# Kernel optimization log

Measured on AMD Instinct MI355X. Metric: run time of the kernel, lower is better.

The kernel has to match this reference:

```python
import jax, jax.numpy as jnp
import numpy as np

NUM_HEADS = 8
BLOCK = 8      # block_size
HALO = 2       # kernel_size (halo width)


def _rel_to_abs(rel):
    # halo-style relative->absolute conversion
    # rel: [B, G, qh, qw, 2*p-1] -> [B, G, qh, qw, p]
    B, G, qh, qw, dim = rel.shape
    p = (dim + 1) // 2
    gap = p - qw
    flat = rel.reshape(B, G, qh, qw * dim)[:, :, :, qw - 1:-1]
    return flat.reshape(B, G, qh, qw, 2 * (p - 1))[:, :, :, :, gap:p + gap]


def _relative_logits(pos_q, pos_emb_h, pos_emb_w):
    # pos_q: [B, G, qb, qb, kd]; pos_emb_*: [kd, 2*p-1]
    rel_w = _rel_to_abs(jnp.einsum('bghwd,dr->bghwr', pos_q, pos_emb_w))  # [B,G,qb,qb,p] key-width
    q_t = pos_q.transpose(0, 1, 3, 2, 4)
    rel_h = _rel_to_abs(jnp.einsum('bgwhd,dr->bgwhr', q_t, pos_emb_h))
    rel_h = rel_h.transpose(0, 1, 3, 2, 4)  # [B,G,qb,qb,p] key-height
    return rel_h[..., :, None] + rel_w[..., None, :]  # [B,G,qb,qb,p,p]


def reference(x, w_q, w_kv, w_out, pos_emb_h, pos_emb_w):
    B, H, W, C = x.shape
    kd = C // NUM_HEADS                # per-head key dim
    kvk = BLOCK + 2 * HALO             # halo window size
    out_ch = w_out.shape[1]
    v_dim = out_ch // NUM_HEADS
    kv_per_head = (C + out_ch) // NUM_HEADS
    hh, ww = H // BLOCK, W // BLOCK
    scale = float(1.0 / np.sqrt(kd))

    # ---- query (1x1 conv == matmul), blockify ----
    q = (x @ w_q).reshape(B, hh, BLOCK, ww, BLOCK, NUM_HEADS, kd)
    q = q.transpose(0, 5, 1, 3, 2, 4, 6)  # [B,nh,hh,ww,qb,qb,kd]
    attn_q = q.reshape(B, NUM_HEADS, hh, ww, BLOCK * BLOCK, kd) * scale
    pos_q = q.reshape(B, NUM_HEADS * hh * ww, BLOCK, BLOCK, kd)

    # ---- key/value: 1x1 conv, halo pad, unfold into overlapping windows ----
    kv = jnp.pad(x @ w_kv, ((0, 0), (HALO, HALO), (HALO, HALO), (0, 0)))
    idx = np.arange(hh)[:, None] * BLOCK + np.arange(kvk)[None, :]  # [hh,kvk]
    idy = np.arange(ww)[:, None] * BLOCK + np.arange(kvk)[None, :]  # [ww,kvk]
    patches = kv[:, idx][:, :, :, idy]           # [B,hh,kvk,ww,kvk,kv_dim]
    patches = patches.transpose(0, 1, 3, 2, 4, 5)  # [B,hh,ww,kvk,kvk,kv_dim]
    kvh = patches.reshape(B, hh, ww, kvk, kvk, NUM_HEADS, kv_per_head)
    kvh = kvh.transpose(0, 5, 1, 2, 3, 4, 6).reshape(B, NUM_HEADS, hh, ww, kvk * kvk, kv_per_head)
    key, value = kvh[..., :kd], kvh[..., kd:]

    # ---- attention with relative position bias ----
    scores = jnp.einsum('bnhwqd,bnhwkd->bnhwqk', attn_q, key)
    pos = _relative_logits(pos_q, pos_emb_h, pos_emb_w)
    pos = pos.reshape(B, NUM_HEADS, hh, ww, BLOCK * BLOCK, kvk * kvk)
    attn = jax.nn.softmax(scores + pos, axis=-1)
    out = jnp.einsum('bnhwqk,bnhwkv->bnhwqv', attn, value)  # [B,nh,hh,ww,qb*qb,v_dim]

    # ---- de-blockify, output projection ----
    out = out.reshape(B, NUM_HEADS, hh, ww, BLOCK, BLOCK, v_dim)
    out = out.transpose(0, 2, 4, 3, 5, 1, 6).reshape(B, H, W, NUM_HEADS * v_dim)
    return out @ w_out


def setup_inputs() -> dict:
    key = jax.random.key(0)
    ks = jax.random.split(key, 6)
    B, H, W, C = 4, 128, 128, 256
    out_ch = 256
    kd = C // NUM_HEADS
    kvk = BLOCK + 2 * HALO
    std = kd ** -0.5
    return {
        'x': jax.random.normal(ks[0], (B, H, W, C), jnp.float32),
        'w_q': jax.random.normal(ks[1], (C, C), jnp.float32) * 0.02,
        'w_kv': jax.random.normal(ks[2], (C, C + out_ch), jnp.float32) * 0.02,
        'w_out': jax.random.normal(ks[3], (C, out_ch), jnp.float32) * 0.02,
        'pos_emb_h': jax.random.normal(ks[4], (kd, 2 * kvk - 1), jnp.float32) * std,
        'pos_emb_w': jax.random.normal(ks[5], (kd, 2 * kvk - 1), jnp.float32) * std,
    }
```

## Files before the change

kernel.cpp:

```cpp
#include <hip/hip_runtime.h>
#include <hip/hip_bf16.h>
#include <cstdint>


#define KVK 12
#define NKEYS 144
#define VT_S 160
#define PT_S 168
#define LOG2E 1.4426950408889634f

typedef unsigned int u32;
typedef unsigned long long u64;
typedef unsigned short u16;
typedef __attribute__((ext_vector_type(8))) __bf16 bf16x8;
typedef __attribute__((ext_vector_type(4))) float f32x4;

__device__ __forceinline__ u16 f2bf(float f) {
    u32 x = __float_as_uint(f);
    return (u16)((x + 0x7fffu + ((x >> 16) & 1u)) >> 16);
}
__device__ __forceinline__ u32 cvtpk(float lo, float hi) {
    u32 d;
    asm("v_cvt_pk_bf16_f32 %0, %1, %2" : "=v"(d) : "v"(lo), "v"(hi));
    return d;
}
__device__ __forceinline__ float max3f(float a, float b, float c) {
    float d;
    asm("v_max3_f32 %0, %1, %2, %3" : "=v"(d) : "v"(a), "v"(b), "v"(c));
    return d;
}
__device__ __forceinline__ float exp2a(float x) {
    float d;
    asm("v_exp_f32 %0, %1" : "=v"(d) : "v"(x));
    return d;
}
__device__ __forceinline__ void gload16(const void* g, void* l) {
    __builtin_amdgcn_global_load_lds(
        (const __attribute__((address_space(1))) void*)g,
        (__attribute__((address_space(3))) void*)l, 16, 0, 0);
}
__device__ __forceinline__ u32 pack2(float lo, float hi) {
    return (u32)f2bf(lo) | ((u32)f2bf(hi) << 16);
}

__global__ __launch_bounds__(256) void conv_prep(const float* __restrict__ x,
                                                 u16* __restrict__ xb,
                                                 const float* __restrict__ wq,
                                                 const float* __restrict__ wkv,
                                                 const float* __restrict__ wout,
                                                 u16* __restrict__ wT,
                                                 u16* __restrict__ woutT,
                                                 const float* __restrict__ emb_h,
                                                 const float* __restrict__ emb_w,
                                                 u16* __restrict__ embT) {
    int blk = blockIdx.x, t = threadIdx.x;
    if (blk < 8192) {
        int i = blk * 256 + t;
        const float4* p = reinterpret_cast<const float4*>(x) + (long)i * 2;
        float4 a = p[0], b = p[1];
        uint4 o;
        o.x = pack2(a.x, a.y); o.y = pack2(a.z, a.w);
        o.z = pack2(b.x, b.y); o.w = pack2(b.z, b.w);
        reinterpret_cast<uint4*>(xb)[i] = o;
        return;
    }
    blk -= 8192;
    if (blk < 256) {
        int idx = blk * 256 + t; int nn = idx >> 8, k = idx & 255;
        wT[idx] = f2bf(wq[(long)k * 256 + nn]);
    } else if (blk < 768) {
        int idx = (blk - 256) * 256 + t; int nn = idx >> 8, k = idx & 255;
        float v = wkv[(long)k * 512 + nn];
        if ((nn & 32) == 0) v *= 0.2550348642f;
        wT[65536 + idx] = f2bf(v);
    } else if (blk < 1024) {
        int idx = (blk - 768) * 256 + t; int nn = idx >> 8, k = idx & 255;
        woutT[idx] = f2bf(wout[(long)k * 256 + nn]);
    } else if (blk == 1024) {
        for (int i = t; i < 1024; i += 256) {
            int p = i >> 5, d = i & 31;
            embT[i] = (p < 23) ? f2bf(emb_h[d * 23 + p]) : 0;
        }
    } else {
        for (int i = t; i < 1024; i += 256) {
            int p = i >> 5, d = i & 31;
            embT[1024 + i] = (p < 23) ? f2bf(emb_w[d * 23 + p]) : 0;
        }
    }
}

__global__ __launch_bounds__(256) void gemm_qkv6(const u16* __restrict__ A,
                                                 const u16* __restrict__ WT,
                                                 u16* __restrict__ Qb,
                                                 u16* __restrict__ KVb) {
    __shared__ u16 As[8192];
    __shared__ u16 Bs[8192];
    const int t = threadIdx.x;
    const int bid = blockIdx.x;
    const int mIdx = (bid / 48) * 8 + (bid & 7);
    const int nt = (bid >> 3) % 6;
    const int w = t >> 6, lane = t & 63;
    const long m0 = (long)mIdx * 128;
    const long n0 = (long)nt * 128;
    const int wr = w >> 1, wc = w & 1;
    const int r = lane & 15, g = lane >> 4;

    f32x4 acc[4][4];
    #pragma unroll
    for (int i = 0; i < 4; ++i)
        #pragma unroll
        for (int j = 0; j < 4; ++j) acc[i][j] = (f32x4){0.f, 0.f, 0.f, 0.f};

    const u16* Ags[4];
    const u16* Bgs[4];
    #pragma unroll
    for (int cq = 0; cq < 4; ++cq) {
        int u = cq * 256 + w * 64 + lane;
        int panel = u >> 9, row = (u >> 2) & 127, col8 = (u & 3) * 8;
        Ags[cq] = A + (m0 + row) * 256 + panel * 32 + col8;
        Bgs[cq] = WT + (n0 + row) * 256 + panel * 32 + col8;
    }

    for (int k0 = 0; k0 < 256; k0 += 64) {
        #pragma unroll
        for (int cq = 0; cq < 4; ++cq) {
            gload16(Ags[cq] + k0, &As[cq * 2048 + w * 512]);
            gload16(Bgs[cq] + k0, &Bs[cq * 2048 + w * 512]);
        }
        __syncthreads();
        #pragma unroll
        for (int kk = 0; kk < 2; ++kk) {
            bf16x8 a[4], b[4];
            #pragma unroll
            for (int i = 0; i < 4; ++i)
                a[i] = *reinterpret_cast<const bf16x8*>(
                    &As[kk * 4096 + (wr * 64 + i * 16 + r) * 32 + g * 8]);
            #pragma unroll
            for (int j = 0; j < 4; ++j)
                b[j] = *reinterpret_cast<const bf16x8*>(
                    &Bs[kk * 4096 + (wc * 64 + j * 16 + r) * 32 + g * 8]);
            #pragma unroll
            for (int i = 0; i < 4; ++i)
                #pragma unroll
                for (int j = 0; j < 4; ++j)
                    acc[i][j] = __builtin_amdgcn_mfma_f32_16x16x32_bf16(b[j], a[i], acc[i][j], 0, 0, 0);
        }
        __syncthreads();
    }

    const bool isQ = (nt < 2);
    #pragma unroll
    for (int i = 0; i < 4; ++i) {
        long row = m0 + wr * 64 + i * 16 + r;
        #pragma unroll
        for (int j = 0; j < 4; ++j) {
            long colb = n0 + wc * 64 + j * 16 + g * 4;
            uint2 st;
            st.x = cvtpk(acc[i][j][0], acc[i][j][1]);
            st.y = cvtpk(acc[i][j][2], acc[i][j][3]);
            if (isQ) *reinterpret_cast<uint2*>(Qb + row * 256 + colb) = st;
            else     *reinterpret_cast<uint2*>(KVb + row * 512 + colb - 256) = st;
        }
    }
}

__global__ __launch_bounds__(256) void mfma_gemm(const u16* __restrict__ A,
                                                 const u16* __restrict__ BT,
                                                 float* __restrict__ C, int N) {
    __shared__ u16 As[8192];
    __shared__ u16 Bs[8192];
    const int t = threadIdx.x;
    const int bid = blockIdx.x;
    const int mIdx = (bid / 16) * 8 + (bid & 7);
    const int nt = (bid >> 3) & 1;
    const int w = t >> 6, lane = t & 63;
    const long m0 = (long)mIdx * 128;
    const long n0 = (long)nt * 128;
    const int wr = w >> 1, wc = w & 1;
    const int r = lane & 15, g = lane >> 4;

    f32x4 acc[4][4];
    #pragma unroll
    for (int i = 0; i < 4; ++i)
        #pragma unroll
        for (int j = 0; j < 4; ++j) acc[i][j] = (f32x4){0.f, 0.f, 0.f, 0.f};

    const u16* Ags[4];
    const u16* Bgs[4];
    #pragma unroll
    for (int cq = 0; cq < 4; ++cq) {
        int u = cq * 256 + w * 64 + lane;
        int panel = u >> 9, row = (u >> 2) & 127, col8 = (u & 3) * 8;
        Ags[cq] = A + (m0 + row) * 256 + panel * 32 + col8;
        Bgs[cq] = BT + (n0 + row) * 256 + panel * 32 + col8;
    }

    for (int k0 = 0; k0 < 256; k0 += 64) {
        #pragma unroll
        for (int cq = 0; cq < 4; ++cq) {
            gload16(Ags[cq] + k0, &As[cq * 2048 + w * 512]);
            gload16(Bgs[cq] + k0, &Bs[cq * 2048 + w * 512]);
        }
        __syncthreads();
        #pragma unroll
        for (int kk = 0; kk < 2; ++kk) {
            bf16x8 a[4], b[4];
            #pragma unroll
            for (int i = 0; i < 4; ++i)
                a[i] = *reinterpret_cast<const bf16x8*>(
                    &As[kk * 4096 + (wr * 64 + i * 16 + r) * 32 + g * 8]);
            #pragma unroll
            for (int j = 0; j < 4; ++j)
                b[j] = *reinterpret_cast<const bf16x8*>(
                    &Bs[kk * 4096 + (wc * 64 + j * 16 + r) * 32 + g * 8]);
            #pragma unroll
            for (int i = 0; i < 4; ++i)
                #pragma unroll
                for (int j = 0; j < 4; ++j)
                    acc[i][j] = __builtin_amdgcn_mfma_f32_16x16x32_bf16(b[j], a[i], acc[i][j], 0, 0, 0);
        }
        __syncthreads();
    }

    #pragma unroll
    for (int i = 0; i < 4; ++i) {
        long row = m0 + wr * 64 + i * 16 + r;
        #pragma unroll
        for (int j = 0; j < 4; ++j) {
            long colb = n0 + wc * 64 + j * 16 + g * 4;
            float4 st = make_float4(acc[i][j][0], acc[i][j][1], acc[i][j][2], acc[i][j][3]);
            *reinterpret_cast<float4*>(C + row * N + colb) = st;
        }
    }
}

__global__ __launch_bounds__(256, 5) void attn_mfma(const u16* __restrict__ Qb,
                                                    const u16* __restrict__ KVb,
                                                    const u16* __restrict__ embT,
                                                    u16* __restrict__ Ob) {
    __shared__ __align__(16) char blob[22528];
    u16* Ks  = (u16*)blob;
    u16* Qe  = (u16*)(blob + 18432);
    u16* PT  = (u16*)blob;
    __shared__ u16 Vt[32 * VT_S];

    const int gblk = blockIdx.x;
    const int n = gblk & 7;
    const int bx = (gblk >> 3) & 15;
    const int by = (gblk >> 7) & 15;
    const int b = gblk >> 11;
    const int t = threadIdx.x;
    const int w = t >> 6, lane = t & 63;
    const int g = lane >> 4, r = lane & 15;

    const int q = w * 16 + r;
    const int qi = q >> 3, qj = q & 7;
    const long qrow = ((long)b * 128 + by * 8 + qi) * 128 + bx * 8 + qj;

    bf16x8 qa1 = *reinterpret_cast<const bf16x8*>(Qb + qrow * 256 + n * 32 + g * 8);

    for (int u = t; u < NKEYS * 8; u += 256) {
        int kk = u >> 3, part = u & 7;
        int ky = kk / KVK, kx = kk - ky * KVK;
        int gy = by * 8 + ky - 2, gx = bx * 8 + kx - 2;
        uint4 val = make_uint4(0u, 0u, 0u, 0u);
        if ((unsigned)gy < 128u && (unsigned)gx < 128u) {
            long row = ((long)b * 128 + gy) * 128 + gx;
            val = *reinterpret_cast<const uint4*>(KVb + row * 512 + n * 64 + part * 8);
        }
        if (part < 4) {
            int col = (part * 8) ^ ((kk & 7) << 3);
            *reinterpret_cast<uint4*>(&Ks[kk * 64 + col]) = val;
        } else {
            int d0 = (part - 4) * 8;
            u16 tmp[8];
            *reinterpret_cast<uint4*>(tmp) = val;
            #pragma unroll
            for (int i = 0; i < 8; ++i) {
                int d = d0 + i;
                Vt[d * VT_S + (kk ^ (((d >> 3) & 3) << 3))] = tmp[i];
            }
        }
    }
    for (int u = t; u < 576; u += 256) {
        int kk = u >> 2, uu = u & 3;
        int ky = (kk * 171) >> 11;
        int kx = kk - 12 * ky;
        int hy = ky - 8 * uu;
        int hx = 12 + kx - 8 * uu;
        u64 lo = 0, hi = 0;
        if ((unsigned)hy < 4u) lo |= 0x3F80ULL << (hy * 16);
        else if ((unsigned)hy < 8u) hi |= 0x3F80ULL << ((hy - 4) * 16);
        if ((unsigned)hx < 4u) lo |= 0x3F80ULL << (hx * 16);
        else if ((unsigned)hx < 8u) hi |= 0x3F80ULL << ((hx - 4) * 16);
        int col = (32 + uu * 8) ^ ((kk & 7) << 3);
        u64* dst = reinterpret_cast<u64*>(&Ks[kk * 64 + col]);
        dst[0] = lo;
        dst[1] = hi;
    }
    if (t < 64) *reinterpret_cast<uint4*>(&Qe[t * 32 + 24]) = make_uint4(0u, 0u, 0u, 0u);
    if (t >= 224) {
        int d = t - 224;
        int sw = ((d >> 3) & 3) << 3;
        *reinterpret_cast<uint4*>(&Vt[d * VT_S + (144 ^ sw)]) = make_uint4(0u, 0u, 0u, 0u);
        *reinterpret_cast<uint4*>(&Vt[d * VT_S + (152 ^ sw)]) = make_uint4(0u, 0u, 0u, 0u);
    }

    {
        bf16x8 ah0 = *reinterpret_cast<const bf16x8*>(embT + r * 32 + g * 8);
        bf16x8 ah1 = *reinterpret_cast<const bf16x8*>(embT + (16 + r) * 32 + g * 8);
        bf16x8 aw0 = *reinterpret_cast<const bf16x8*>(embT + 1024 + r * 32 + g * 8);
        bf16x8 aw1 = *reinterpret_cast<const bf16x8*>(embT + 1024 + (16 + r) * 32 + g * 8);
        f32x4 z = (f32x4){0.f, 0.f, 0.f, 0.f};
        f32x4 rh0 = __builtin_amdgcn_mfma_f32_16x16x32_bf16(ah0, qa1, z, 0, 0, 0);
        f32x4 rh1 = __builtin_amdgcn_mfma_f32_16x16x32_bf16(ah1, qa1, z, 0, 0, 0);
        f32x4 rw0 = __builtin_amdgcn_mfma_f32_16x16x32_bf16(aw0, qa1, z, 0, 0, 0);
        f32x4 rw1 = __builtin_amdgcn_mfma_f32_16x16x32_bf16(aw1, qa1, z, 0, 0, 0);
        #pragma unroll
        for (int ti = 0; ti < 2; ++ti) {
            #pragma unroll
            for (int e = 0; e < 4; ++e) {
                int p = ti * 16 + g * 4 + e;
                float vh = (ti ? rh1[e] : rh0[e]) * LOG2E;
                float vw = (ti ? rw1[e] : rw0[e]) * LOG2E;
                int kyd = p + qi - 11;
                int kxd = p + qj - 11;
                if ((unsigned)kyd < 12u) Qe[q * 32 + kyd] = f2bf(vh);
                if ((unsigned)kxd < 12u) Qe[q * 32 + 12 + kxd] = f2bf(vw);
            }
        }
    }
    __syncthreads();

    bf16x8 qa2 = *reinterpret_cast<const bf16x8*>(&Qe[q * 32 + g * 8]);
    f32x4 acc[9];
    #pragma unroll
    for (int j = 0; j < 9; ++j) {
        int krow = j * 16 + r;
        int sw = (r & 7) << 3;
        bf16x8 kb0 = *reinterpret_cast<const bf16x8*>(&Ks[krow * 64 + ((g * 8) ^ sw)]);
        bf16x8 kb1 = *reinterpret_cast<const bf16x8*>(&Ks[krow * 64 + ((32 + g * 8) ^ sw)]);
        f32x4 z = (f32x4){0.f, 0.f, 0.f, 0.f};
        acc[j] = __builtin_amdgcn_mfma_f32_16x16x32_bf16(kb1, qa2,
                 __builtin_amdgcn_mfma_f32_16x16x32_bf16(kb0, qa1, z, 0, 0, 0), 0, 0, 0);
    }

    float mx = max3f(acc[0][0], acc[0][1], acc[0][2]);
    mx = fmaxf(mx, acc[0][3]);
    #pragma unroll
    for (int j = 1; j < 9; ++j)
        mx = max3f(mx, max3f(acc[j][0], acc[j][1], acc[j][2]), acc[j][3]);
    mx = fmaxf(mx, __shfl_xor(mx, 16));
    mx = fmaxf(mx, __shfl_xor(mx, 32));
    float s0 = 0.f, s1 = 0.f, s2 = 0.f, s3 = 0.f;
    u32 pkA[9], pkB[9];
    #pragma unroll
    for (int j = 0; j < 9; ++j) {
        float e0 = exp2a(acc[j][0] - mx);
        float e1 = exp2a(acc[j][1] - mx);
        float e2 = exp2a(acc[j][2] - mx);
        float e3 = exp2a(acc[j][3] - mx);
        s0 += e0; s1 += e1; s2 += e2; s3 += e3;
        pkA[j] = cvtpk(e0, e1);
        pkB[j] = cvtpk(e2, e3);
    }
    float sum = (s0 + s1) + (s2 + s3);
    sum += __shfl_xor(sum, 16);
    sum += __shfl_xor(sum, 32);
    const float inv = __builtin_amdgcn_rcpf(sum);

    __syncthreads();

    {
        const int ptb = q * PT_S;
        #pragma unroll
        for (int j = 0; j < 9; ++j) {
            *reinterpret_cast<u32*>(&PT[ptb + 16 * j + 4 * g]) = pkA[j];
            *reinterpret_cast<u32*>(&PT[ptb + 16 * j + 4 * g + 2]) = pkB[j];
        }
    }
    if (t < 64) {
        *reinterpret_cast<uint4*>(&PT[t * PT_S + 144]) = make_uint4(0u, 0u, 0u, 0u);
        *reinterpret_cast<uint4*>(&PT[t * PT_S + 152]) = make_uint4(0u, 0u, 0u, 0u);
    }
    __syncthreads();

    const int sw0 = (r >> 3) << 3;
    const int sw1 = (2 + (r >> 3)) << 3;
    f32x4 o0 = (f32x4){0.f, 0.f, 0.f, 0.f};
    f32x4 o1 = (f32x4){0.f, 0.f, 0.f, 0.f};
    #pragma unroll
    for (int kk = 0; kk < 5; ++kk) {
        bf16x8 pb = *reinterpret_cast<const bf16x8*>(&PT[q * PT_S + kk * 32 + g * 8]);
        bf16x8 va0 = *reinterpret_cast<const bf16x8*>(&Vt[r * VT_S + ((kk * 32 + g * 8) ^ sw0)]);
        bf16x8 va1 = *reinterpret_cast<const bf16x8*>(&Vt[(16 + r) * VT_S + ((kk * 32 + g * 8) ^ sw1)]);
        o0 = __builtin_amdgcn_mfma_f32_16x16x32_bf16(va0, pb, o0, 0, 0, 0);
        o1 = __builtin_amdgcn_mfma_f32_16x16x32_bf16(va1, pb, o1, 0, 0, 0);
    }
    {
        uint2 st0, st1;
        st0.x = cvtpk(o0[0] * inv, o0[1] * inv);
        st0.y = cvtpk(o0[2] * inv, o0[3] * inv);
        st1.x = cvtpk(o1[0] * inv, o1[1] * inv);
        st1.y = cvtpk(o1[2] * inv, o1[3] * inv);
        *reinterpret_cast<uint2*>(Ob + qrow * 256 + n * 32 + g * 4) = st0;
        *reinterpret_cast<uint2*>(Ob + qrow * 256 + n * 32 + 16 + g * 4) = st1;
    }
}

extern "C" void kernel_launch(void* const* d_in, const int* in_sizes, int n_in,
                              void* d_out, int out_size, void* d_ws, size_t ws_size,
                              hipStream_t stream) {
    const float* x     = (const float*)d_in[0];
    const float* w_q   = (const float*)d_in[1];
    const float* w_kv  = (const float*)d_in[2];
    const float* w_out = (const float*)d_in[3];
    const float* emb_h = (const float*)d_in[4];
    const float* emb_w = (const float*)d_in[5];

    u16* xb = (u16*)d_out;
    u16* Qb = (u16*)((char*)d_out + (size_t)33554432);
    char* ws = (char*)d_ws;
    u16* KVb   = (u16*)(ws);
    u16* Ob    = (u16*)(ws + (size_t)67108864);
    u16* wT    = (u16*)(ws + (size_t)100663296);
    u16* woutT = (u16*)(ws + (size_t)100663296 + 393216);
    u16* embT  = (u16*)(ws + (size_t)100663296 + 524288);

    dim3 blk(256);
    conv_prep<<<dim3(9218), blk, 0, stream>>>(x, xb, w_q, w_kv, w_out, wT, woutT,
                                              emb_h, emb_w, embT);
    gemm_qkv6<<<dim3(3072), blk, 0, stream>>>(xb, wT, Qb, KVb);
    attn_mfma<<<dim3(8192), blk, 0, stream>>>(Qb, KVb, embT, Ob);
    mfma_gemm<<<dim3(1024), blk, 0, stream>>>(Ob, woutT, (float*)d_out, 256);
}
```

Measured before the change: 146.5 us.

## Issue all KV gathers up front and defer V scatter behind positional MFMAs

The KV window load is restructured so each thread issues all its global loads (key and value halves together) up front into registers, stores K immediately, and defers the V transpose-scatter until after the relative-position MFMA work. The embedding loads are hoisted to the kernel start. s_setprio brackets are added around the MFMA sections so waves doing matrix math get scheduling priority. The goal is to hide global-load latency behind independent compute; the cost is more live registers under a launch bound of 5 blocks per SM.

```diff
diff --git a/kernel.cpp b/kernel.cpp
--- a/kernel.cpp
+++ b/kernel.cpp
@@ -234,6 +234,25 @@
     }
 }
 
+#define UNITLOAD(U, VK, VV, KD, VB) {                                          \
+    int kk_ = (U) >> 2, p_ = (U) & 3;                                          \
+    int ky_ = (kk_ * 171) >> 11, kx_ = kk_ - 12 * ky_;                         \
+    int gy_ = by * 8 + ky_ - 2, gx_ = bx * 8 + kx_ - 2;                        \
+    if (((unsigned)gy_ < 128u) && ((unsigned)gx_ < 128u)) {                    \
+        const u16* bp_ = KVb + (((long)b * 128 + gy_) * 128 + gx_) * 512 + n * 64 + p_ * 8; \
+        VK = *reinterpret_cast<const uint4*>(bp_);                             \
+        VV = *reinterpret_cast<const uint4*>(bp_ + 32);                        \
+    }                                                                          \
+    KD = kk_ * 64 + ((p_ * 8) ^ ((kk_ & 7) << 3));                             \
+    VB = (p_ * 8) * VT_S + (kk_ ^ (p_ << 3));                                  \
+}
+#define VSCAT(VV, VB) {                                                        \
+    u16 tmp_[8];                                                               \
+    *reinterpret_cast<uint4*>(tmp_) = VV;                                      \
+    _Pragma("unroll")                                                          \
+    for (int i_ = 0; i_ < 8; ++i_) Vt[(VB) + i_ * VT_S] = tmp_[i_];            \
+}
+
 __global__ __launch_bounds__(256, 5) void attn_mfma(const u16* __restrict__ Qb,
                                                     const u16* __restrict__ KVb,
                                                     const u16* __restrict__ embT,
@@ -258,30 +277,22 @@
     const long qrow = ((long)b * 128 + by * 8 + qi) * 128 + bx * 8 + qj;
 
     bf16x8 qa1 = *reinterpret_cast<const bf16x8*>(Qb + qrow * 256 + n * 32 + g * 8);
-
-    for (int u = t; u < NKEYS * 8; u += 256) {
-        int kk = u >> 3, part = u & 7;
-        int ky = kk / KVK, kx = kk - ky * KVK;
-        int gy = by * 8 + ky - 2, gx = bx * 8 + kx - 2;
-        uint4 val = make_uint4(0u, 0u, 0u, 0u);
-        if ((unsigned)gy < 128u && (unsigned)gx < 128u) {
-            long row = ((long)b * 128 + gy) * 128 + gx;
-            val = *reinterpret_cast<const uint4*>(KVb + row * 512 + n * 64 + part * 8);
-        }
-        if (part < 4) {
-            int col = (part * 8) ^ ((kk & 7) << 3);
-            *reinterpret_cast<uint4*>(&Ks[kk * 64 + col]) = val;
-        } else {
-            int d0 = (part - 4) * 8;
-            u16 tmp[8];
-            *reinterpret_cast<uint4*>(tmp) = val;
-            #pragma unroll
-            for (int i = 0; i < 8; ++i) {
-                int d = d0 + i;
-                Vt[d * VT_S + (kk ^ (((d >> 3) & 3) << 3))] = tmp[i];
-            }
-        }
-    }
+    bf16x8 ah0 = *reinterpret_cast<const bf16x8*>(embT + r * 32 + g * 8);
+    bf16x8 ah1 = *reinterpret_cast<const bf16x8*>(embT + (16 + r) * 32 + g * 8);
+    bf16x8 aw0 = *reinterpret_cast<const bf16x8*>(embT + 1024 + r * 32 + g * 8);
+    bf16x8 aw1 = *reinterpret_cast<const bf16x8*>(embT + 1024 + (16 + r) * 32 + g * 8);
+
+    uint4 z4 = make_uint4(0u, 0u, 0u, 0u);
+    uint4 vK0 = z4, vV0 = z4, vK1 = z4, vV1 = z4, vK2 = z4, vV2 = z4;
+    int kd0 = 0, vb0 = 0, kd1 = 0, vb1 = 0, kd2 = 0, vb2 = 0;
+    UNITLOAD(t, vK0, vV0, kd0, vb0);
+    UNITLOAD(t + 256, vK1, vV1, kd1, vb1);
+    if (t < 64) UNITLOAD(t + 512, vK2, vV2, kd2, vb2);
+
+    *reinterpret_cast<uint4*>(&Ks[kd0]) = vK0;
+    *reinterpret_cast<uint4*>(&Ks[kd1]) = vK1;
+    if (t < 64) *reinterpret_cast<uint4*>(&Ks[kd2]) = vK2;
+
     for (int u = t; u < 576; u += 256) {
         int kk = u >> 2, uu = u & 3;
         int ky = (kk * 171) >> 11;
@@ -298,24 +309,22 @@
         dst[0] = lo;
         dst[1] = hi;
     }
-    if (t < 64) *reinterpret_cast<uint4*>(&Qe[t * 32 + 24]) = make_uint4(0u, 0u, 0u, 0u);
+    if (t < 64) *reinterpret_cast<uint4*>(&Qe[t * 32 + 24]) = z4;
     if (t >= 224) {
         int d = t - 224;
         int sw = ((d >> 3) & 3) << 3;
-        *reinterpret_cast<uint4*>(&Vt[d * VT_S + (144 ^ sw)]) = make_uint4(0u, 0u, 0u, 0u);
-        *reinterpret_cast<uint4*>(&Vt[d * VT_S + (152 ^ sw)]) = make_uint4(0u, 0u, 0u, 0u);
+        *reinterpret_cast<uint4*>(&Vt[d * VT_S + (144 ^ sw)]) = z4;
+        *reinterpret_cast<uint4*>(&Vt[d * VT_S + (152 ^ sw)]) = z4;
     }
 
     {
-        bf16x8 ah0 = *reinterpret_cast<const bf16x8*>(embT + r * 32 + g * 8);
-        bf16x8 ah1 = *reinterpret_cast<const bf16x8*>(embT + (16 + r) * 32 + g * 8);
-        bf16x8 aw0 = *reinterpret_cast<const bf16x8*>(embT + 1024 + r * 32 + g * 8);
-        bf16x8 aw1 = *reinterpret_cast<const bf16x8*>(embT + 1024 + (16 + r) * 32 + g * 8);
         f32x4 z = (f32x4){0.f, 0.f, 0.f, 0.f};
+        __builtin_amdgcn_s_setprio(1);
         f32x4 rh0 = __builtin_amdgcn_mfma_f32_16x16x32_bf16(ah0, qa1, z, 0, 0, 0);
         f32x4 rh1 = __builtin_amdgcn_mfma_f32_16x16x32_bf16(ah1, qa1, z, 0, 0, 0);
         f32x4 rw0 = __builtin_amdgcn_mfma_f32_16x16x32_bf16(aw0, qa1, z, 0, 0, 0);
         f32x4 rw1 = __builtin_amdgcn_mfma_f32_16x16x32_bf16(aw1, qa1, z, 0, 0, 0);
+        __builtin_amdgcn_s_setprio(0);
         #pragma unroll
         for (int ti = 0; ti < 2; ++ti) {
             #pragma unroll
@@ -330,10 +339,16 @@
             }
         }
     }
+
+    VSCAT(vV0, vb0);
+    VSCAT(vV1, vb1);
+    if (t < 64) VSCAT(vV2, vb2);
+
     __syncthreads();
 
     bf16x8 qa2 = *reinterpret_cast<const bf16x8*>(&Qe[q * 32 + g * 8]);
     f32x4 acc[9];
+    __builtin_amdgcn_s_setprio(1);
     #pragma unroll
     for (int j = 0; j < 9; ++j) {
         int krow = j * 16 + r;
@@ -344,6 +359,7 @@
         acc[j] = __builtin_amdgcn_mfma_f32_16x16x32_bf16(kb1, qa2,
                  __builtin_amdgcn_mfma_f32_16x16x32_bf16(kb0, qa1, z, 0, 0, 0), 0, 0, 0);
     }
+    __builtin_amdgcn_s_setprio(0);
 
     float mx = max3f(acc[0][0], acc[0][1], acc[0][2]);
     mx = fmaxf(mx, acc[0][3]);
@@ -389,6 +405,7 @@
     const int sw1 = (2 + (r >> 3)) << 3;
     f32x4 o0 = (f32x4){0.f, 0.f, 0.f, 0.f};
     f32x4 o1 = (f32x4){0.f, 0.f, 0.f, 0.f};
+    __builtin_amdgcn_s_setprio(1);
     #pragma unroll
     for (int kk = 0; kk < 5; ++kk) {
         bf16x8 pb = *reinterpret_cast<const bf16x8*>(&PT[q * PT_S + kk * 32 + g * 8]);
@@ -397,6 +414,7 @@
         o0 = __builtin_amdgcn_mfma_f32_16x16x32_bf16(va0, pb, o0, 0, 0, 0);
         o1 = __builtin_amdgcn_mfma_f32_16x16x32_bf16(va1, pb, o1, 0, 0, 0);
     }
+    __builtin_amdgcn_s_setprio(0);
     {
         uint2 st0, st1;
         st0.x = cvtpk(o0[0] * inv, o0[1] * inv);
```

Measured after the change: 132.9 us. 9.3% less time.
